# Kernel tuning notes

Measured on AMD Instinct MI355X. Metric: run time of the kernel, lower is better.

The kernel has to match this reference:

```python
import jax, jax.numpy as jnp
import numpy as np

B, S, HID = 4, 2048, 512
NH, HD = 8, 64
MAX_REL = 512


def setup_inputs() -> dict:
    key = jax.random.key(0)
    ks = jax.random.split(key, 10)
    sd = 0.02
    return {
        "hidden_states": jax.random.normal(ks[0], (B, S, HID), jnp.float32),
        "attention_mask": jnp.ones((B, S), jnp.float32),
        "Wq": jax.random.normal(ks[1], (HID, HID), jnp.float32) * sd,
        "bq": jnp.zeros((HID,), jnp.float32),
        "Wk": jax.random.normal(ks[2], (HID, HID), jnp.float32) * sd,
        "bk": jnp.zeros((HID,), jnp.float32),
        "Wv": jax.random.normal(ks[3], (HID, HID), jnp.float32) * sd,
        "bv": jnp.zeros((HID,), jnp.float32),
        "Wo": jax.random.normal(ks[4], (HID, HID), jnp.float32) * sd,
        "bo": jnp.zeros((HID,), jnp.float32),
        "rel_table": jax.random.normal(ks[5], (2 * MAX_REL + 1, NH), jnp.float32) * sd,
    }


def _heads(x):
    # [B,S,HID] -> [B,NH,S,HD]
    return x.reshape(B, S, NH, HD).transpose(0, 2, 1, 3)


def reference(hidden_states, attention_mask, Wq, bq, Wk, bk, Wv, bv, Wo, bo, rel_table):
    q = _heads(hidden_states @ Wq + bq)
    k = _heads(hidden_states @ Wk + bk)
    v = _heads(hidden_states @ Wv + bv)

    scores = jnp.einsum("bhqd,bhkd->bhqk", q, k) / jnp.sqrt(jnp.float32(HD))

    # relative position bias: rel[i,j] = clip(j-i, -MAX_REL, MAX_REL) + MAX_REL
    pos = jnp.arange(S)
    rel = jnp.clip(pos[None, :] - pos[:, None], -MAX_REL, MAX_REL) + MAX_REL
    bias = rel_table[rel]                      # [S,S,NH]
    bias = bias.transpose(2, 0, 1)             # [NH,S,S]
    scores = scores + bias[None]

    # mask: 1 attend, 0 masked
    neg = jnp.finfo(scores.dtype).min
    scores = scores + (1.0 - attention_mask)[:, None, None, :] * neg

    probs = jax.nn.softmax(scores, axis=-1)
    ctx = jnp.einsum("bhqk,bhkd->bhqd", probs, v)
    ctx = ctx.transpose(0, 2, 1, 3).reshape(B, S, HID)
    return ctx @ Wo + bo
```

## Files before the change

### kernel.cpp

```cpp
#include <hip/hip_runtime.h>
#include <hip/hip_bf16.h>

#define B_    4
#define S_    2048
#define HID_  512
#define NH_   8
#define HD_   64
#define MAXREL 512
#define M_    (B_ * S_)

#define LOG2E 1.44269504f
#define SCALE_Q (0.125f * LOG2E)

typedef __attribute__((ext_vector_type(8))) short bf8;
typedef __attribute__((ext_vector_type(4))) float f4;
typedef __attribute__((ext_vector_type(16))) float f16f;

static __device__ __forceinline__ unsigned short f2bf(float f) {
    union { float f; unsigned int u; } v; v.f = f;
    unsigned int u = v.u;
    unsigned int r = (u + 0x7FFFu + ((u >> 16) & 1u)) >> 16;
    return (unsigned short)r;
}

static __device__ __forceinline__ float ex2(float x) {
    float r; asm("v_exp_f32 %0, %1" : "=v"(r) : "v"(x)); return r;
}

static __device__ __forceinline__ void gload16(const void* g, void* l) {
    __builtin_amdgcn_global_load_lds(
        (const __attribute__((address_space(1))) unsigned int*)g,
        (__attribute__((address_space(3))) unsigned int*)l, 16, 0, 0);
}

static __device__ __forceinline__ bf8 mkbf8(unsigned a, unsigned b, unsigned c, unsigned d) {
    uint4 u = make_uint4(a, b, c, d);
    return *(bf8*)&u;
}

#define MFMA16(a, b, c) __builtin_amdgcn_mfma_f32_16x16x32_bf16((a), (b), (c), 0, 0, 0)
#define MFMA32(a, b, c) __builtin_amdgcn_mfma_f32_32x32x16_bf16((a), (b), (c), 0, 0, 0)

__global__ void k_cast_hs(const float* __restrict__ src, unsigned short* __restrict__ dst, int n4) {
    int i = blockIdx.x * blockDim.x + threadIdx.x;
    if (i >= n4) return;
    float4 v = ((const float4*)src)[i];
    ushort4 o;
    o.x = f2bf(v.x); o.y = f2bf(v.y); o.z = f2bf(v.z); o.w = f2bf(v.w);
    ((ushort4*)dst)[i] = o;
}

__global__ void k_prep_mask(const float* __restrict__ mask, float* __restrict__ maskadd) {
    int i = blockIdx.x * blockDim.x + threadIdx.x;
    if (i < M_) maskadd[i] = (1.0f - mask[i]) * -3.0e38f;
}

__global__ void k_transpose_w4(const float* __restrict__ W0, const float* __restrict__ W1,
                               const float* __restrict__ W2, const float* __restrict__ W3,
                               unsigned short* __restrict__ T0, unsigned short* __restrict__ T1,
                               unsigned short* __restrict__ T2, unsigned short* __restrict__ T3) {
    __shared__ float tile[32][33];
    const int z = blockIdx.z;
    const float* W = (z == 0) ? W0 : (z == 1) ? W1 : (z == 2) ? W2 : W3;
    unsigned short* T = (z == 0) ? T0 : (z == 1) ? T1 : (z == 2) ? T2 : T3;
    const int tx = threadIdx.x & 31, ty = threadIdx.x >> 5;
    const int n0 = blockIdx.x * 32, k0 = blockIdx.y * 32;
    #pragma unroll
    for (int i = 0; i < 4; ++i)
        tile[ty + i * 8][tx] = W[(size_t)(k0 + ty + i * 8) * HID_ + n0 + tx];
    __syncthreads();
    #pragma unroll
    for (int i = 0; i < 4; ++i)
        T[(size_t)(n0 + ty + i * 8) * HID_ + k0 + tx] = f2bf(tile[tx][ty + i * 8]);
}

__global__ __launch_bounds__(256, 3) void k_gemm_qkv(
    const unsigned short* __restrict__ Abf,
    const unsigned short* __restrict__ Wqt, const unsigned short* __restrict__ Wkt,
    const unsigned short* __restrict__ Wvt,
    const float* __restrict__ bq, const float* __restrict__ bk, const float* __restrict__ bv,
    unsigned short* __restrict__ Q, unsigned short* __restrict__ K, unsigned short* __restrict__ Vt)
{
    __shared__ unsigned short Al[2][128 * 32];
    __shared__ unsigned short Bl[2][128 * 32];

    const int t = threadIdx.x;
    const int lane = t & 63, w = t >> 6;
    const int lr = lane & 15, lg = lane >> 4;
    const int wr = w >> 1, wc = w & 1;

    const int m0 = blockIdx.x * 128;
    const int ng = blockIdx.y * 128;
    const int z = ng >> 9;
    const int n0 = ng & 511;
    const unsigned short* Wt = (z == 0) ? Wqt : ((z == 1) ? Wkt : Wvt);
    const float* bias = (z == 0) ? bq : ((z == 1) ? bk : bv);
    const float osc = (z == 0) ? SCALE_Q : 1.0f;

    const int srow = t >> 2;
    const int sc = (((t & 3) ^ ((srow >> 1) & 3))) * 8;
    const unsigned short* Ag0 = &Abf[(size_t)(m0 + srow) * HID_ + sc];
    const unsigned short* Ag1 = &Abf[(size_t)(m0 + 64 + srow) * HID_ + sc];
    const unsigned short* Bg0 = &Wt[(size_t)(n0 + srow) * HID_ + sc];
    const unsigned short* Bg1 = &Wt[(size_t)(n0 + 64 + srow) * HID_ + sc];
    char* dA0 = (char*)&Al[0][0] + w * 1024;
    char* dB0 = (char*)&Bl[0][0] + w * 1024;

    const int fx = (lr >> 1) & 3;
    int aoff[4], boff[4];
    #pragma unroll
    for (int i = 0; i < 4; ++i) {
        aoff[i] = (wr * 64 + i * 16 + lr) * 32 + ((lg ^ fx) * 8);
        boff[i] = (wc * 64 + i * 16 + lr) * 32 + ((lg ^ fx) * 8);
    }

    gload16(Ag0, dA0);
    gload16(Ag1, dA0 + 4096);
    gload16(Bg0, dB0);
    gload16(Bg1, dB0 + 4096);
    __syncthreads();

    f4 acc[4][4] = {};
    for (int kt = 0; kt < 16; ++kt) {
        const int cur = kt & 1;
        if (kt < 15) {
            const int ko = (kt + 1) * 32;
            const int bo = (cur ^ 1) * 8192;
            gload16(Ag0 + ko, dA0 + bo);
            gload16(Ag1 + ko, dA0 + bo + 4096);
            gload16(Bg0 + ko, dB0 + bo);
            gload16(Bg1 + ko, dB0 + bo + 4096);
        }
        bf8 af[4], bf_[4];
        #pragma unroll
        for (int i = 0; i < 4; ++i) {
            af[i]  = *(const bf8*)&Al[cur][aoff[i]];
            bf_[i] = *(const bf8*)&Bl[cur][boff[i]];
        }
        #pragma unroll
        for (int mi = 0; mi < 4; ++mi)
            #pragma unroll
            for (int ni = 0; ni < 4; ++ni)
                acc[mi][ni] = MFMA16(af[mi], bf_[ni], acc[mi][ni]);
        __syncthreads();
    }

    #pragma unroll
    for (int mi = 0; mi < 4; ++mi)
    #pragma unroll
    for (int ni = 0; ni < 4; ++ni) {
        const int col = n0 + wc * 64 + ni * 16 + lr;
        const int h = col >> 6, d = col & 63;
        const float bs = bias[col];
        const int row0 = m0 + wr * 64 + mi * 16 + lg * 4;
        const int b = row0 >> 11, s0 = row0 & 2047;
        if (z == 2) {
            ushort4 o;
            o.x = f2bf(acc[mi][ni][0] + bs);
            o.y = f2bf(acc[mi][ni][1] + bs);
            o.z = f2bf(acc[mi][ni][2] + bs);
            o.w = f2bf(acc[mi][ni][3] + bs);
            *(ushort4*)&Vt[(((size_t)(b * NH_ + h)) * HD_ + d) * S_ + s0] = o;
        } else {
            unsigned short* dst = (z == 0) ? Q : K;
            #pragma unroll
            for (int r = 0; r < 4; ++r) {
                float v = (acc[mi][ni][r] + bs) * osc;
                dst[(((size_t)(b * NH_ + h)) * S_ + s0 + r) * HD_ + d] = f2bf(v);
            }
        }
    }
}

__global__ __launch_bounds__(512) void k_gemm_out(
    const unsigned short* __restrict__ Abf,
    const unsigned short* __restrict__ Wot,
    const float* __restrict__ bo,
    float* __restrict__ out)
{
    __shared__ unsigned short Al[2][128 * 32];
    __shared__ unsigned short Bl[2][128 * 32];

    const int t = threadIdx.x;
    const int lane = t & 63, w = t >> 6;
    const int lr = lane & 15, lg = lane >> 4;
    const int wr = w >> 2, wc = w & 3;

    const int m0 = blockIdx.x * 128;
    const int n0 = blockIdx.y * 128;

    const int srow = t >> 2;
    const int sc = (((t & 3) ^ ((srow >> 1) & 3))) * 8;
    const unsigned short* Ag = &Abf[(size_t)(m0 + srow) * HID_ + sc];
    const unsigned short* Bg = &Wot[(size_t)(n0 + srow) * HID_ + sc];
    char* dA = (char*)&Al[0][0] + w * 1024;
    char* dB = (char*)&Bl[0][0] + w * 1024;

    const int fx = (lr >> 1) & 3;
    int aoff[4], boff[2];
    #pragma unroll
    for (int i = 0; i < 4; ++i)
        aoff[i] = (wr * 64 + i * 16 + lr) * 32 + ((lg ^ fx) * 8);
    #pragma unroll
    for (int i = 0; i < 2; ++i)
        boff[i] = (wc * 32 + i * 16 + lr) * 32 + ((lg ^ fx) * 8);

    gload16(Ag, dA);
    gload16(Bg, dB);
    __syncthreads();

    f4 acc[4][2] = {};
    for (int kt = 0; kt < 16; ++kt) {
        const int cur = kt & 1;
        if (kt < 15) {
            const int ko = (kt + 1) * 32;
            const int bo_ = (cur ^ 1) * 8192;
            gload16(Ag + ko, dA + bo_);
            gload16(Bg + ko, dB + bo_);
        }
        bf8 af[4], bf_[2];
        #pragma unroll
        for (int i = 0; i < 4; ++i) af[i] = *(const bf8*)&Al[cur][aoff[i]];
        #pragma unroll
        for (int i = 0; i < 2; ++i) bf_[i] = *(const bf8*)&Bl[cur][boff[i]];
        #pragma unroll
        for (int mi = 0; mi < 4; ++mi)
            #pragma unroll
            for (int ni = 0; ni < 2; ++ni)
                acc[mi][ni] = MFMA16(af[mi], bf_[ni], acc[mi][ni]);
        __syncthreads();
    }

    #pragma unroll
    for (int mi = 0; mi < 4; ++mi)
    #pragma unroll
    for (int ni = 0; ni < 2; ++ni) {
        const int col = n0 + wc * 32 + ni * 16 + lr;
        const float bs = bo[col];
        const int row0 = m0 + wr * 64 + mi * 16 + lg * 4;
        #pragma unroll
        for (int r = 0; r < 4; ++r)
            out[(size_t)(row0 + r) * HID_ + col] = acc[mi][ni][r] + bs;
    }
}

__global__ __launch_bounds__(256, 2) void k_flash(
    const unsigned short* __restrict__ Q, const unsigned short* __restrict__ K,
    const unsigned short* __restrict__ Vt,
    const float* __restrict__ rel_table, const float* __restrict__ maskadd,
    unsigned short* __restrict__ ctx)
{
    __shared__ unsigned short KV[3][8192];
    __shared__ float Tbp[2176];
    __shared__ float maskc[S_];

    const int t = threadIdx.x;
    const int lane = t & 63, w = t >> 6;
    const int q = lane & 31, hi = lane >> 5;

    const int flat = blockIdx.x;
    const int idx = flat >> 3;
    const int bh = (flat & 7) * 4 + (idx >> 4);
    const int qb = idx & 15;
    const int b = bh >> 3, h = bh & 7;
    const int q0 = qb * 128;

    for (int i = t; i < 2176; i += 256) {
        int r = i - q0 - 127;
        r = r < -MAXREL ? -MAXREL : (r > MAXREL ? MAXREL : r);
        Tbp[i] = rel_table[(r + MAXREL) * NH_ + h] * LOG2E;
    }
    {
        const float4* src = (const float4*)(maskadd + b * S_);
        float4* dst = (float4*)maskc;
        for (int i = t; i < S_ / 4; i += 256) dst[i] = src[i];
    }
    const float TbLo = rel_table[h] * LOG2E;
    const float TbHi = rel_table[2 * MAXREL * NH_ + h] * LOG2E;

    const unsigned short* Kb = K + (size_t)bh * S_ * HD_;
    const unsigned short* Vb = Vt + (size_t)bh * HD_ * S_;

    const int myq = q0 + w * 32 + q;
    const int qw = q0 + w * 32;
    bf8 qf[4];
    #pragma unroll
    for (int s = 0; s < 4; ++s)
        qf[s] = *(const bf8*)&Q[((size_t)bh * S_ + myq) * HD_ + s * 16 + hi * 8];

    const int srow = t >> 3, sslot = t & 7;
    const int sxor = (sslot ^ (srow & 7)) * 8;
    const size_t kb0 = (size_t)srow * HD_ + sxor;
    const size_t kb1 = (size_t)(srow + 32) * HD_ + sxor;
    const size_t vb0 = (size_t)srow * S_ + sxor;
    const size_t vb1 = (size_t)(srow + 32) * S_ + sxor;
    const int woff = w * 1024;

    auto stage = [&](int kvt, int buf) {
        char* base = (char*)&KV[buf][0];
        const size_t ko = (size_t)kvt * 64 * HD_;
        const size_t vo = (size_t)kvt * 64;
        gload16(&Kb[kb0 + ko], base + woff);
        gload16(&Kb[kb1 + ko], base + 4096 + woff);
        gload16(&Vb[vb0 + vo], base + 8192 + woff);
        gload16(&Vb[vb1 + vo], base + 8192 + 4096 + woff);
    };

    f16f ca0 = {}, ca1 = {};
    float m_s = -INFINITY, lsum = 0.f;

    stage(0, 0);
    stage(1, 1);
    asm volatile("s_waitcnt lgkmcnt(0)" ::: "memory");
    asm volatile("s_waitcnt vmcnt(4)" ::: "memory");
    __builtin_amdgcn_s_barrier();
    __builtin_amdgcn_sched_barrier(0);

    const int xq = q & 7;
    const int jb0 = 127 - w * 32 - q + 4 * hi;
    int cur = 0;
    for (int ti = 0; ti < 32; ++ti) {
        const int kv0 = ti * 64;

        if (ti < 30) {
            int nb = cur + 2; if (nb >= 3) nb -= 3;
            stage(ti + 2, nb);
        }
        const unsigned short* Kt  = &KV[cur][0];
        const unsigned short* Vtl = &KV[cur][4096];

        f16f sa0 = {}, sa1 = {};
        __builtin_amdgcn_s_setprio(1);
        #pragma unroll
        for (int s = 0; s < 4; ++s) {
            const int slot = ((2 * s + hi) ^ xq) * 8;
            bf8 k0 = *(const bf8*)&Kt[q * 64 + slot];
            bf8 k1 = *(const bf8*)&Kt[(q + 32) * 64 + slot];
            sa0 = MFMA32(k0, qf[s], sa0);
            sa1 = MFMA32(k1, qf[s], sa1);
        }
        __builtin_amdgcn_s_setprio(0);

        float tmaxl = -INFINITY;
        {
            const bool ulo = (kv0 + 31 - qw <= -MAXREL);
            const bool uhi = (kv0 - (qw + 31) >= MAXREL);
            if (ulo || uhi) {
                const float bc = ulo ? TbLo : TbHi;
                #pragma unroll
                for (int m = 0; m < 4; ++m) {
                    float4 mk = *(const float4*)&maskc[kv0 + m * 8 + hi * 4];
                    #pragma unroll
                    for (int r = 0; r < 4; ++r) {
                        float mkv = (r == 0) ? mk.x : (r == 1) ? mk.y : (r == 2) ? mk.z : mk.w;
                        float sv = sa0[4 * m + r] + bc + mkv;
                        sa0[4 * m + r] = sv;
                        tmaxl = fmaxf(tmaxl, sv);
                    }
                }
            } else {
                #pragma unroll
                for (int m = 0; m < 4; ++m) {
                    float4 mk = *(const float4*)&maskc[kv0 + m * 8 + hi * 4];
                    #pragma unroll
                    for (int r = 0; r < 4; ++r) {
                        float mkv = (r == 0) ? mk.x : (r == 1) ? mk.y : (r == 2) ? mk.z : mk.w;
                        float sv = sa0[4 * m + r] + Tbp[jb0 + kv0 + m * 8 + r] + mkv;
                        sa0[4 * m + r] = sv;
                        tmaxl = fmaxf(tmaxl, sv);
                    }
                }
            }
            const int kvh = kv0 + 32;
            const bool ulo1 = (kvh + 31 - qw <= -MAXREL);
            const bool uhi1 = (kvh - (qw + 31) >= MAXREL);
            if (ulo1 || uhi1) {
                const float bc = ulo1 ? TbLo : TbHi;
                #pragma unroll
                for (int m = 0; m < 4; ++m) {
                    float4 mk = *(const float4*)&maskc[kvh + m * 8 + hi * 4];
                    #pragma unroll
                    for (int r = 0; r < 4; ++r) {
                        float mkv = (r == 0) ? mk.x : (r == 1) ? mk.y : (r == 2) ? mk.z : mk.w;
                        float sv = sa1[4 * m + r] + bc + mkv;
                        sa1[4 * m + r] = sv;
                        tmaxl = fmaxf(tmaxl, sv);
                    }
                }
            } else {
                #pragma unroll
                for (int m = 0; m < 4; ++m) {
                    float4 mk = *(const float4*)&maskc[kvh + m * 8 + hi * 4];
                    #pragma unroll
                    for (int r = 0; r < 4; ++r) {
                        float mkv = (r == 0) ? mk.x : (r == 1) ? mk.y : (r == 2) ? mk.z : mk.w;
                        float sv = sa1[4 * m + r] + Tbp[jb0 + kvh + m * 8 + r] + mkv;
                        sa1[4 * m + r] = sv;
                        tmaxl = fmaxf(tmaxl, sv);
                    }
                }
            }
        }
        const float tmax = fmaxf(tmaxl, __shfl_xor(tmaxl, 32));

        float ptile = 0.f;
        unsigned int pkA[8], pkB[8];
        #pragma unroll
        for (int m = 0; m < 4; ++m) {
            float a0 = ex2(sa0[4 * m + 0] - m_s), a1 = ex2(sa0[4 * m + 1] - m_s);
            float a2 = ex2(sa0[4 * m + 2] - m_s), a3 = ex2(sa0[4 * m + 3] - m_s);
            float b0 = ex2(sa1[4 * m + 0] - m_s), b1 = ex2(sa1[4 * m + 1] - m_s);
            float b2 = ex2(sa1[4 * m + 2] - m_s), b3 = ex2(sa1[4 * m + 3] - m_s);
            ptile += ((a0 + a1) + (a2 + a3)) + ((b0 + b1) + (b2 + b3));
            asm("v_cvt_pk_bf16_f32 %0, %1, %2" : "=v"(pkA[2 * m])     : "v"(a0), "v"(a1));
            asm("v_cvt_pk_bf16_f32 %0, %1, %2" : "=v"(pkA[2 * m + 1]) : "v"(a2), "v"(a3));
            asm("v_cvt_pk_bf16_f32 %0, %1, %2" : "=v"(pkB[2 * m])     : "v"(b0), "v"(b1));
            asm("v_cvt_pk_bf16_f32 %0, %1, %2" : "=v"(pkB[2 * m + 1]) : "v"(b2), "v"(b3));
        }
        if (!__all(tmax <= m_s + 8.0f)) {
            const float mnew = fmaxf(m_s, tmax);
            const float fac = ex2(m_s - mnew);
            lsum *= fac;
            ca0 *= fac;
            ca1 *= fac;
            ptile = 0.f;
            #pragma unroll
            for (int m = 0; m < 4; ++m) {
                float a0 = ex2(sa0[4 * m + 0] - mnew), a1 = ex2(sa0[4 * m + 1] - mnew);
                float a2 = ex2(sa0[4 * m + 2] - mnew), a3 = ex2(sa0[4 * m + 3] - mnew);
                float b0 = ex2(sa1[4 * m + 0] - mnew), b1 = ex2(sa1[4 * m + 1] - mnew);
                float b2 = ex2(sa1[4 * m + 2] - mnew), b3 = ex2(sa1[4 * m + 3] - mnew);
                ptile += ((a0 + a1) + (a2 + a3)) + ((b0 + b1) + (b2 + b3));
                asm("v_cvt_pk_bf16_f32 %0, %1, %2" : "=v"(pkA[2 * m])     : "v"(a0), "v"(a1));
                asm("v_cvt_pk_bf16_f32 %0, %1, %2" : "=v"(pkA[2 * m + 1]) : "v"(a2), "v"(a3));
                asm("v_cvt_pk_bf16_f32 %0, %1, %2" : "=v"(pkB[2 * m])     : "v"(b0), "v"(b1));
                asm("v_cvt_pk_bf16_f32 %0, %1, %2" : "=v"(pkB[2 * m + 1]) : "v"(b2), "v"(b3));
            }
            m_s = mnew;
        }
        lsum += ptile;

        bf8 pf[4];
        #pragma unroll
        for (int s2 = 0; s2 < 2; ++s2) {
            unsigned c0 = pkA[4 * s2],     c2 = pkA[4 * s2 + 2];
            unsigned c1 = pkA[4 * s2 + 1], c3 = pkA[4 * s2 + 3];
            asm("v_permlane32_swap_b32 %0, %1" : "+v"(c0), "+v"(c2));
            asm("v_permlane32_swap_b32 %0, %1" : "+v"(c1), "+v"(c3));
            pf[s2] = mkbf8(c0, c1, c2, c3);
        }
        #pragma unroll
        for (int s2 = 0; s2 < 2; ++s2) {
            unsigned c0 = pkB[4 * s2],     c2 = pkB[4 * s2 + 2];
            unsigned c1 = pkB[4 * s2 + 1], c3 = pkB[4 * s2 + 3];
            asm("v_permlane32_swap_b32 %0, %1" : "+v"(c0), "+v"(c2));
            asm("v_permlane32_swap_b32 %0, %1" : "+v"(c1), "+v"(c3));
            pf[2 + s2] = mkbf8(c0, c1, c2, c3);
        }

        __builtin_amdgcn_s_setprio(1);
        #pragma unroll
        for (int s = 0; s < 4; ++s) {
            const int slot = ((2 * s + hi) ^ xq) * 8;
            bf8 v0 = *(const bf8*)&Vtl[q * 64 + slot];
            bf8 v1 = *(const bf8*)&Vtl[(q + 32) * 64 + slot];
            ca0 = MFMA32(v0, pf[s], ca0);
            ca1 = MFMA32(v1, pf[s], ca1);
        }
        __builtin_amdgcn_s_setprio(0);

        if (ti < 31) {
            if (ti < 30) asm volatile("s_waitcnt vmcnt(4)" ::: "memory");
            else         asm volatile("s_waitcnt vmcnt(0)" ::: "memory");
            __builtin_amdgcn_s_barrier();
            __builtin_amdgcn_sched_barrier(0);
        }
        cur = (cur == 2) ? 0 : cur + 1;
    }

    lsum += __shfl_xor(lsum, 32);
    const float inv = 1.0f / lsum;
    unsigned short* cg = &ctx[(size_t)(b * S_ + myq) * HID_ + h * HD_];
    #pragma unroll
    for (int m = 0; m < 4; ++m) {
        ushort4 o0;
        o0.x = f2bf(ca0[4 * m + 0] * inv);
        o0.y = f2bf(ca0[4 * m + 1] * inv);
        o0.z = f2bf(ca0[4 * m + 2] * inv);
        o0.w = f2bf(ca0[4 * m + 3] * inv);
        *(ushort4*)&cg[m * 8 + hi * 4] = o0;
        ushort4 o1;
        o1.x = f2bf(ca1[4 * m + 0] * inv);
        o1.y = f2bf(ca1[4 * m + 1] * inv);
        o1.z = f2bf(ca1[4 * m + 2] * inv);
        o1.w = f2bf(ca1[4 * m + 3] * inv);
        *(ushort4*)&cg[32 + m * 8 + hi * 4] = o1;
    }
}

extern "C" void kernel_launch(void* const* d_in, const int* in_sizes, int n_in,
                              void* d_out, int out_size, void* d_ws, size_t ws_size,
                              hipStream_t stream) {
    const float* hs  = (const float*)d_in[0];
    const float* msk = (const float*)d_in[1];
    const float* Wq  = (const float*)d_in[2];
    const float* bq  = (const float*)d_in[3];
    const float* Wk  = (const float*)d_in[4];
    const float* bk  = (const float*)d_in[5];
    const float* Wv  = (const float*)d_in[6];
    const float* bv  = (const float*)d_in[7];
    const float* Wo  = (const float*)d_in[8];
    const float* bo  = (const float*)d_in[9];
    const float* rel = (const float*)d_in[10];
    float* out = (float*)d_out;

    char* ws = (char*)d_ws;
    unsigned short* hsb = (unsigned short*)ws; ws += (size_t)M_ * HID_ * 2;
    unsigned short* Wqt = (unsigned short*)ws; ws += (size_t)HID_ * HID_ * 2;
    unsigned short* Wkt = (unsigned short*)ws; ws += (size_t)HID_ * HID_ * 2;
    unsigned short* Wvt = (unsigned short*)ws; ws += (size_t)HID_ * HID_ * 2;
    unsigned short* Wot = (unsigned short*)ws; ws += (size_t)HID_ * HID_ * 2;
    unsigned short* Qb  = (unsigned short*)ws; ws += (size_t)M_ * HID_ * 2;
    unsigned short* Kb  = (unsigned short*)ws; ws += (size_t)M_ * HID_ * 2;
    unsigned short* Vtb = (unsigned short*)ws; ws += (size_t)M_ * HID_ * 2;
    unsigned short* ctxb= (unsigned short*)ws; ws += (size_t)M_ * HID_ * 2;
    float* maskadd      = (float*)ws;          ws += (size_t)M_ * 4;

    k_cast_hs<<<(M_ * HID_ / 4 + 255) / 256, 256, 0, stream>>>(hs, hsb, M_ * HID_ / 4);
    k_prep_mask<<<(M_ + 255) / 256, 256, 0, stream>>>(msk, maskadd);
    k_transpose_w4<<<dim3(16, 16, 4), 256, 0, stream>>>(Wq, Wk, Wv, Wo, Wqt, Wkt, Wvt, Wot);
    k_gemm_qkv<<<dim3(64, 12), 256, 0, stream>>>(
        hsb, Wqt, Wkt, Wvt, bq, bk, bv, Qb, Kb, Vtb);
    k_flash<<<512, 256, 0, stream>>>(Qb, Kb, Vtb, rel, maskadd, ctxb);
    k_gemm_out<<<dim3(64, 4), 512, 0, stream>>>(ctxb, Wot, bo, out);
}
```

Measured before the change: 111.8 us.

## Software-pipeline PV MFMA one tile behind QK with a four-buffer KV ring

The P·V matrix multiply for tile ti-1 is deferred into iteration ti, issued right after the Q·K MFMAs. This lets the softmax work of one tile overlap matrix-core work from another, instead of serialising QK, softmax and PV inside each tile. The KV shared ring grows from three to four buffers so the previous V tile stays resident, and a tail block finishes the last PV. The relative-bias table is shrunk to a fixed 1216-entry window, and the row-max reduction is split into four independent chains to shorten dependency latency. The larger shared-memory footprint (~77KB per block) sits close to the per-CU limit at two blocks per CU.

After: 112.4 us. Within noise of the previous version (+0.5%).

```diff
diff --git a/kernel.cpp b/kernel.cpp
--- a/kernel.cpp
+++ b/kernel.cpp
@@ -250,8 +250,8 @@
     const float* __restrict__ rel_table, const float* __restrict__ maskadd,
     unsigned short* __restrict__ ctx)
 {
-    __shared__ unsigned short KV[3][8192];
-    __shared__ float Tbp[2176];
+    __shared__ unsigned short KV[4][8192];
+    __shared__ float Tw[1216];
     __shared__ float maskc[S_];
 
     const int t = threadIdx.x;
@@ -265,10 +265,10 @@
     const int b = bh >> 3, h = bh & 7;
     const int q0 = qb * 128;
 
-    for (int i = t; i < 2176; i += 256) {
-        int r = i - q0 - 127;
+    for (int i = t; i < 1216; i += 256) {
+        int r = i - 606;
         r = r < -MAXREL ? -MAXREL : (r > MAXREL ? MAXREL : r);
-        Tbp[i] = rel_table[(r + MAXREL) * NH_ + h] * LOG2E;
+        Tw[i] = rel_table[(r + MAXREL) * NH_ + h] * LOG2E;
     }
     {
         const float4* src = (const float4*)(maskadd + b * S_);
@@ -308,6 +308,8 @@
 
     f16f ca0 = {}, ca1 = {};
     float m_s = -INFINITY, lsum = 0.f;
+    bf8 pfA, pfB, pfC, pfD;
+    pfA = pfB = pfC = pfD = bf8{};
 
     stage(0, 0);
     stage(1, 1);
@@ -317,17 +319,14 @@
     __builtin_amdgcn_sched_barrier(0);
 
     const int xq = q & 7;
-    const int jb0 = 127 - w * 32 - q + 4 * hi;
-    int cur = 0;
+    const int jb0 = 606 - q0 - w * 32 - q + 4 * hi;
     for (int ti = 0; ti < 32; ++ti) {
         const int kv0 = ti * 64;
-
-        if (ti < 30) {
-            int nb = cur + 2; if (nb >= 3) nb -= 3;
-            stage(ti + 2, nb);
-        }
-        const unsigned short* Kt  = &KV[cur][0];
-        const unsigned short* Vtl = &KV[cur][4096];
+        const int cur = ti & 3;
+
+        if (ti < 30) stage(ti + 2, (ti + 2) & 3);
+
+        const unsigned short* Kt = &KV[cur][0];
 
         f16f sa0 = {}, sa1 = {};
         __builtin_amdgcn_s_setprio(1);
@@ -339,9 +338,21 @@
             sa0 = MFMA32(k0, qf[s], sa0);
             sa1 = MFMA32(k1, qf[s], sa1);
         }
+        if (ti > 0) {
+            const unsigned short* Vp = &KV[(ti + 3) & 3][4096];
+            #pragma unroll
+            for (int s = 0; s < 4; ++s) {
+                const int slot = ((2 * s + hi) ^ xq) * 8;
+                bf8 v0 = *(const bf8*)&Vp[q * 64 + slot];
+                bf8 v1 = *(const bf8*)&Vp[(q + 32) * 64 + slot];
+                bf8 pf = (s == 0) ? pfA : (s == 1) ? pfB : (s == 2) ? pfC : pfD;
+                ca0 = MFMA32(v0, pf, ca0);
+                ca1 = MFMA32(v1, pf, ca1);
+            }
+        }
         __builtin_amdgcn_s_setprio(0);
 
-        float tmaxl = -INFINITY;
+        float t0 = -INFINITY, t1 = -INFINITY, t2 = -INFINITY, t3 = -INFINITY;
         {
             const bool ulo = (kv0 + 31 - qw <= -MAXREL);
             const bool uhi = (kv0 - (qw + 31) >= MAXREL);
@@ -350,25 +361,20 @@
                 #pragma unroll
                 for (int m = 0; m < 4; ++m) {
                     float4 mk = *(const float4*)&maskc[kv0 + m * 8 + hi * 4];
-                    #pragma unroll
-                    for (int r = 0; r < 4; ++r) {
-                        float mkv = (r == 0) ? mk.x : (r == 1) ? mk.y : (r == 2) ? mk.z : mk.w;
-                        float sv = sa0[4 * m + r] + bc + mkv;
-                        sa0[4 * m + r] = sv;
-                        tmaxl = fmaxf(tmaxl, sv);
-                    }
+                    float s0 = sa0[4 * m + 0] + bc + mk.x;  sa0[4 * m + 0] = s0;  t0 = fmaxf(t0, s0);
+                    float s1 = sa0[4 * m + 1] + bc + mk.y;  sa0[4 * m + 1] = s1;  t1 = fmaxf(t1, s1);
+                    float s2 = sa0[4 * m + 2] + bc + mk.z;  sa0[4 * m + 2] = s2;  t2 = fmaxf(t2, s2);
+                    float s3 = sa0[4 * m + 3] + bc + mk.w;  sa0[4 * m + 3] = s3;  t3 = fmaxf(t3, s3);
                 }
             } else {
                 #pragma unroll
                 for (int m = 0; m < 4; ++m) {
                     float4 mk = *(const float4*)&maskc[kv0 + m * 8 + hi * 4];
-                    #pragma unroll
-                    for (int r = 0; r < 4; ++r) {
-                        float mkv = (r == 0) ? mk.x : (r == 1) ? mk.y : (r == 2) ? mk.z : mk.w;
-                        float sv = sa0[4 * m + r] + Tbp[jb0 + kv0 + m * 8 + r] + mkv;
-                        sa0[4 * m + r] = sv;
-                        tmaxl = fmaxf(tmaxl, sv);
-                    }
+                    const int jb = jb0 + kv0 + m * 8;
+                    float s0 = sa0[4 * m + 0] + Tw[jb + 0] + mk.x;  sa0[4 * m + 0] = s0;  t0 = fmaxf(t0, s0);
+                    float s1 = sa0[4 * m + 1] + Tw[jb + 1] + mk.y;  sa0[4 * m + 1] = s1;  t1 = fmaxf(t1, s1);
+                    float s2 = sa0[4 * m + 2] + Tw[jb + 2] + mk.z;  sa0[4 * m + 2] = s2;  t2 = fmaxf(t2, s2);
+                    float s3 = sa0[4 * m + 3] + Tw[jb + 3] + mk.w;  sa0[4 * m + 3] = s3;  t3 = fmaxf(t3, s3);
                 }
             }
             const int kvh = kv0 + 32;
@@ -379,28 +385,24 @@
                 #pragma unroll
                 for (int m = 0; m < 4; ++m) {
                     float4 mk = *(const float4*)&maskc[kvh + m * 8 + hi * 4];
-                    #pragma unroll
-                    for (int r = 0; r < 4; ++r) {
-                        float mkv = (r == 0) ? mk.x : (r == 1) ? mk.y : (r == 2) ? mk.z : mk.w;
-                        float sv = sa1[4 * m + r] + bc + mkv;
-                        sa1[4 * m + r] = sv;
-                        tmaxl = fmaxf(tmaxl, sv);
-                    }
+                    float s0 = sa1[4 * m + 0] + bc + mk.x;  sa1[4 * m + 0] = s0;  t0 = fmaxf(t0, s0);
+                    float s1 = sa1[4 * m + 1] + bc + mk.y;  sa1[4 * m + 1] = s1;  t1 = fmaxf(t1, s1);
+                    float s2 = sa1[4 * m + 2] + bc + mk.z;  sa1[4 * m + 2] = s2;  t2 = fmaxf(t2, s2);
+                    float s3 = sa1[4 * m + 3] + bc + mk.w;  sa1[4 * m + 3] = s3;  t3 = fmaxf(t3, s3);
                 }
             } else {
                 #pragma unroll
                 for (int m = 0; m < 4; ++m) {
                     float4 mk = *(const float4*)&maskc[kvh + m * 8 + hi * 4];
-                    #pragma unroll
-                    for (int r = 0; r < 4; ++r) {
-                        float mkv = (r == 0) ? mk.x : (r == 1) ? mk.y : (r == 2) ? mk.z : mk.w;
-                        float sv = sa1[4 * m + r] + Tbp[jb0 + kvh + m * 8 + r] + mkv;
-                        sa1[4 * m + r] = sv;
-                        tmaxl = fmaxf(tmaxl, sv);
-                    }
+                    const int jb = jb0 + kvh + m * 8;
+                    float s0 = sa1[4 * m + 0] + Tw[jb + 0] + mk.x;  sa1[4 * m + 0] = s0;  t0 = fmaxf(t0, s0);
+                    float s1 = sa1[4 * m + 1] + Tw[jb + 1] + mk.y;  sa1[4 * m + 1] = s1;  t1 = fmaxf(t1, s1);
+                    float s2 = sa1[4 * m + 2] + Tw[jb + 2] + mk.z;  sa1[4 * m + 2] = s2;  t2 = fmaxf(t2, s2);
+                    float s3 = sa1[4 * m + 3] + Tw[jb + 3] + mk.w;  sa1[4 * m + 3] = s3;  t3 = fmaxf(t3, s3);
                 }
             }
         }
+        float tmaxl = fmaxf(fmaxf(t0, t1), fmaxf(t2, t3));
         const float tmax = fmaxf(tmaxl, __shfl_xor(tmaxl, 32));
 
         float ptile = 0.f;
@@ -440,34 +442,30 @@
         }
         lsum += ptile;
 
-        bf8 pf[4];
-        #pragma unroll
-        for (int s2 = 0; s2 < 2; ++s2) {
-            unsigned c0 = pkA[4 * s2],     c2 = pkA[4 * s2 + 2];
-            unsigned c1 = pkA[4 * s2 + 1], c3 = pkA[4 * s2 + 3];
+        {
+            unsigned c0 = pkA[0], c2 = pkA[2], c1 = pkA[1], c3 = pkA[3];
             asm("v_permlane32_swap_b32 %0, %1" : "+v"(c0), "+v"(c2));
             asm("v_permlane32_swap_b32 %0, %1" : "+v"(c1), "+v"(c3));
-            pf[s2] = mkbf8(c0, c1, c2, c3);
-        }
-        #pragma unroll
-        for (int s2 = 0; s2 < 2; ++s2) {
-            unsigned c0 = pkB[4 * s2],     c2 = pkB[4 * s2 + 2];
-            unsigned c1 = pkB[4 * s2 + 1], c3 = pkB[4 * s2 + 3];
+            pfA = mkbf8(c0, c1, c2, c3);
+        }
+        {
+            unsigned c0 = pkA[4], c2 = pkA[6], c1 = pkA[5], c3 = pkA[7];
             asm("v_permlane32_swap_b32 %0, %1" : "+v"(c0), "+v"(c2));
             asm("v_permlane32_swap_b32 %0, %1" : "+v"(c1), "+v"(c3));
-            pf[2 + s2] = mkbf8(c0, c1, c2, c3);
-        }
-
-        __builtin_amdgcn_s_setprio(1);
-        #pragma unroll
-        for (int s = 0; s < 4; ++s) {
-            const int slot = ((2 * s + hi) ^ xq) * 8;
-            bf8 v0 = *(const bf8*)&Vtl[q * 64 + slot];
-            bf8 v1 = *(const bf8*)&Vtl[(q + 32) * 64 + slot];
-            ca0 = MFMA32(v0, pf[s], ca0);
-            ca1 = MFMA32(v1, pf[s], ca1);
-        }
-        __builtin_amdgcn_s_setprio(0);
+            pfB = mkbf8(c0, c1, c2, c3);
+        }
+        {
+            unsigned c0 = pkB[0], c2 = pkB[2], c1 = pkB[1], c3 = pkB[3];
+            asm("v_permlane32_swap_b32 %0, %1" : "+v"(c0), "+v"(c2));
+            asm("v_permlane32_swap_b32 %0, %1" : "+v"(c1), "+v"(c3));
+            pfC = mkbf8(c0, c1, c2, c3);
+        }
+        {
+            unsigned c0 = pkB[4], c2 = pkB[6], c1 = pkB[5], c3 = pkB[7];
+            asm("v_permlane32_swap_b32 %0, %1" : "+v"(c0), "+v"(c2));
+            asm("v_permlane32_swap_b32 %0, %1" : "+v"(c1), "+v"(c3));
+            pfD = mkbf8(c0, c1, c2, c3);
+        }
 
         if (ti < 31) {
             if (ti < 30) asm volatile("s_waitcnt vmcnt(4)" ::: "memory");
@@ -475,7 +473,21 @@
             __builtin_amdgcn_s_barrier();
             __builtin_amdgcn_sched_barrier(0);
         }
-        cur = (cur == 2) ? 0 : cur + 1;
+    }
+
+    {
+        const unsigned short* Vp = &KV[3][4096];
+        __builtin_amdgcn_s_setprio(1);
+        #pragma unroll
+        for (int s = 0; s < 4; ++s) {
+            const int slot = ((2 * s + hi) ^ xq) * 8;
+            bf8 v0 = *(const bf8*)&Vp[q * 64 + slot];
+            bf8 v1 = *(const bf8*)&Vp[(q + 32) * 64 + slot];
+            bf8 pf = (s == 0) ? pfA : (s == 1) ? pfB : (s == 2) ? pfC : pfD;
+            ca0 = MFMA32(v0, pf, ca0);
+            ca1 = MFMA32(v1, pf, ca1);
+        }
+        __builtin_amdgcn_s_setprio(0);
     }
 
     lsum += __shfl_xor(lsum, 32);
```

## Split KV tile across two wave groups in flash attention with final LSE merge

Applied to the files above, without the earlier changes.

The flash kernel goes from 4 to 8 waves per block. Each pair of waves shares the same 32 queries but handles a different 32-key half of every 64-key tile, and the two partial softmax states are merged through shared memory at the end. The relative-bias table is shrunk to a window that does not depend on the query block. The goal is more waves in flight to hide latency and a shorter serial chain per wave. The costs are an extra merge step with two block-wide barriers, and the launch bound asks for 4 blocks per CU, which limits registers per thread.

Result: no change. 110.5 us (-1.1%).

```diff
diff --git a/kernel.cpp b/kernel.cpp
--- a/kernel.cpp
+++ b/kernel.cpp
@@ -244,19 +244,20 @@
     }
 }
 
-__global__ __launch_bounds__(256, 2) void k_flash(
+__global__ __launch_bounds__(512, 4) void k_flash(
     const unsigned short* __restrict__ Q, const unsigned short* __restrict__ K,
     const unsigned short* __restrict__ Vt,
     const float* __restrict__ rel_table, const float* __restrict__ maskadd,
     unsigned short* __restrict__ ctx)
 {
     __shared__ unsigned short KV[3][8192];
-    __shared__ float Tbp[2176];
+    __shared__ float Tw[1216];
     __shared__ float maskc[S_];
 
     const int t = threadIdx.x;
     const int lane = t & 63, w = t >> 6;
     const int q = lane & 31, hi = lane >> 5;
+    const int g = w & 3, kvh = w >> 2;
 
     const int flat = blockIdx.x;
     const int idx = flat >> 3;
@@ -265,15 +266,15 @@
     const int b = bh >> 3, h = bh & 7;
     const int q0 = qb * 128;
 
-    for (int i = t; i < 2176; i += 256) {
-        int r = i - q0 - 127;
+    for (int i = t; i < 1216; i += 512) {
+        int r = i - 606;
         r = r < -MAXREL ? -MAXREL : (r > MAXREL ? MAXREL : r);
-        Tbp[i] = rel_table[(r + MAXREL) * NH_ + h] * LOG2E;
+        Tw[i] = rel_table[(r + MAXREL) * NH_ + h] * LOG2E;
     }
     {
         const float4* src = (const float4*)(maskadd + b * S_);
         float4* dst = (float4*)maskc;
-        for (int i = t; i < S_ / 4; i += 256) dst[i] = src[i];
+        for (int i = t; i < S_ / 4; i += 512) dst[i] = src[i];
     }
     const float TbLo = rel_table[h] * LOG2E;
     const float TbHi = rel_table[2 * MAXREL * NH_ + h] * LOG2E;
@@ -281,8 +282,8 @@
     const unsigned short* Kb = K + (size_t)bh * S_ * HD_;
     const unsigned short* Vb = Vt + (size_t)bh * HD_ * S_;
 
-    const int myq = q0 + w * 32 + q;
-    const int qw = q0 + w * 32;
+    const int myq = q0 + g * 32 + q;
+    const int qw = q0 + g * 32;
     bf8 qf[4];
     #pragma unroll
     for (int s = 0; s < 4; ++s)
@@ -291,19 +292,13 @@
     const int srow = t >> 3, sslot = t & 7;
     const int sxor = (sslot ^ (srow & 7)) * 8;
     const size_t kb0 = (size_t)srow * HD_ + sxor;
-    const size_t kb1 = (size_t)(srow + 32) * HD_ + sxor;
     const size_t vb0 = (size_t)srow * S_ + sxor;
-    const size_t vb1 = (size_t)(srow + 32) * S_ + sxor;
     const int woff = w * 1024;
 
     auto stage = [&](int kvt, int buf) {
         char* base = (char*)&KV[buf][0];
-        const size_t ko = (size_t)kvt * 64 * HD_;
-        const size_t vo = (size_t)kvt * 64;
-        gload16(&Kb[kb0 + ko], base + woff);
-        gload16(&Kb[kb1 + ko], base + 4096 + woff);
-        gload16(&Vb[vb0 + vo], base + 8192 + woff);
-        gload16(&Vb[vb1 + vo], base + 8192 + 4096 + woff);
+        gload16(&Kb[kb0 + (size_t)kvt * 64 * HD_], base + woff);
+        gload16(&Vb[vb0 + (size_t)kvt * 64], base + 8192 + woff);
     };
 
     f16f ca0 = {}, ca1 = {};
@@ -312,110 +307,69 @@
     stage(0, 0);
     stage(1, 1);
     asm volatile("s_waitcnt lgkmcnt(0)" ::: "memory");
-    asm volatile("s_waitcnt vmcnt(4)" ::: "memory");
+    asm volatile("s_waitcnt vmcnt(2)" ::: "memory");
     __builtin_amdgcn_s_barrier();
     __builtin_amdgcn_sched_barrier(0);
 
     const int xq = q & 7;
-    const int jb0 = 127 - w * 32 - q + 4 * hi;
-    int cur = 0;
+    const int jb0 = 606 + 32 * kvh + 4 * hi - q0 - g * 32 - q;
     for (int ti = 0; ti < 32; ++ti) {
         const int kv0 = ti * 64;
-
-        if (ti < 30) {
-            int nb = cur + 2; if (nb >= 3) nb -= 3;
-            stage(ti + 2, nb);
-        }
+        const int cur = ti % 3;
+        const int kvs = kv0 + 32 * kvh;
+
+        if (ti < 30) stage(ti + 2, (ti + 2) % 3);
+
         const unsigned short* Kt  = &KV[cur][0];
         const unsigned short* Vtl = &KV[cur][4096];
 
-        f16f sa0 = {}, sa1 = {};
+        f16f sa = {};
         __builtin_amdgcn_s_setprio(1);
         #pragma unroll
         for (int s = 0; s < 4; ++s) {
-            const int slot = ((2 * s + hi) ^ xq) * 8;
-            bf8 k0 = *(const bf8*)&Kt[q * 64 + slot];
-            bf8 k1 = *(const bf8*)&Kt[(q + 32) * 64 + slot];
-            sa0 = MFMA32(k0, qf[s], sa0);
-            sa1 = MFMA32(k1, qf[s], sa1);
+            bf8 kf = *(const bf8*)&Kt[(32 * kvh + q) * 64 + (((2 * s + hi) ^ xq) * 8)];
+            sa = MFMA32(kf, qf[s], sa);
         }
         __builtin_amdgcn_s_setprio(0);
 
-        float tmaxl = -INFINITY;
+        float t0 = -INFINITY, t1 = -INFINITY, t2 = -INFINITY, t3 = -INFINITY;
         {
-            const bool ulo = (kv0 + 31 - qw <= -MAXREL);
-            const bool uhi = (kv0 - (qw + 31) >= MAXREL);
+            const bool ulo = (kvs + 31 - qw <= -MAXREL);
+            const bool uhi = (kvs - (qw + 31) >= MAXREL);
             if (ulo || uhi) {
                 const float bc = ulo ? TbLo : TbHi;
                 #pragma unroll
                 for (int m = 0; m < 4; ++m) {
-                    float4 mk = *(const float4*)&maskc[kv0 + m * 8 + hi * 4];
-                    #pragma unroll
-                    for (int r = 0; r < 4; ++r) {
-                        float mkv = (r == 0) ? mk.x : (r == 1) ? mk.y : (r == 2) ? mk.z : mk.w;
-                        float sv = sa0[4 * m + r] + bc + mkv;
-                        sa0[4 * m + r] = sv;
-                        tmaxl = fmaxf(tmaxl, sv);
-                    }
+                    float4 mk = *(const float4*)&maskc[kvs + m * 8 + hi * 4];
+                    float s0 = sa[4 * m + 0] + bc + mk.x;  sa[4 * m + 0] = s0;  t0 = fmaxf(t0, s0);
+                    float s1 = sa[4 * m + 1] + bc + mk.y;  sa[4 * m + 1] = s1;  t1 = fmaxf(t1, s1);
+                    float s2 = sa[4 * m + 2] + bc + mk.z;  sa[4 * m + 2] = s2;  t2 = fmaxf(t2, s2);
+                    float s3 = sa[4 * m + 3] + bc + mk.w;  sa[4 * m + 3] = s3;  t3 = fmaxf(t3, s3);
                 }
             } else {
                 #pragma unroll
                 for (int m = 0; m < 4; ++m) {
-                    float4 mk = *(const float4*)&maskc[kv0 + m * 8 + hi * 4];
-                    #pragma unroll
-                    for (int r = 0; r < 4; ++r) {
-                        float mkv = (r == 0) ? mk.x : (r == 1) ? mk.y : (r == 2) ? mk.z : mk.w;
-                        float sv = sa0[4 * m + r] + Tbp[jb0 + kv0 + m * 8 + r] + mkv;
-                        sa0[4 * m + r] = sv;
-                        tmaxl = fmaxf(tmaxl, sv);
-                    }
+                    float4 mk = *(const float4*)&maskc[kvs + m * 8 + hi * 4];
+                    const int jb = jb0 + kv0 + m * 8;
+                    float s0 = sa[4 * m + 0] + Tw[jb + 0] + mk.x;  sa[4 * m + 0] = s0;  t0 = fmaxf(t0, s0);
+                    float s1 = sa[4 * m + 1] + Tw[jb + 1] + mk.y;  sa[4 * m + 1] = s1;  t1 = fmaxf(t1, s1);
+                    float s2 = sa[4 * m + 2] + Tw[jb + 2] + mk.z;  sa[4 * m + 2] = s2;  t2 = fmaxf(t2, s2);
+                    float s3 = sa[4 * m + 3] + Tw[jb + 3] + mk.w;  sa[4 * m + 3] = s3;  t3 = fmaxf(t3, s3);
                 }
             }
-            const int kvh = kv0 + 32;
-            const bool ulo1 = (kvh + 31 - qw <= -MAXREL);
-            const bool uhi1 = (kvh - (qw + 31) >= MAXREL);
-            if (ulo1 || uhi1) {
-                const float bc = ulo1 ? TbLo : TbHi;
-                #pragma unroll
-                for (int m = 0; m < 4; ++m) {
-                    float4 mk = *(const float4*)&maskc[kvh + m * 8 + hi * 4];
-                    #pragma unroll
-                    for (int r = 0; r < 4; ++r) {
-                        float mkv = (r == 0) ? mk.x : (r == 1) ? mk.y : (r == 2) ? mk.z : mk.w;
-                        float sv = sa1[4 * m + r] + bc + mkv;
-                        sa1[4 * m + r] = sv;
-                        tmaxl = fmaxf(tmaxl, sv);
-                    }
-                }
-            } else {
-                #pragma unroll
-                for (int m = 0; m < 4; ++m) {
-                    float4 mk = *(const float4*)&maskc[kvh + m * 8 + hi * 4];
-                    #pragma unroll
-                    for (int r = 0; r < 4; ++r) {
-                        float mkv = (r == 0) ? mk.x : (r == 1) ? mk.y : (r == 2) ? mk.z : mk.w;
-                        float sv = sa1[4 * m + r] + Tbp[jb0 + kvh + m * 8 + r] + mkv;
-                        sa1[4 * m + r] = sv;
-                        tmaxl = fmaxf(tmaxl, sv);
-                    }
-                }
-            }
-        }
+        }
+        float tmaxl = fmaxf(fmaxf(t0, t1), fmaxf(t2, t3));
         const float tmax = fmaxf(tmaxl, __shfl_xor(tmaxl, 32));
 
         float ptile = 0.f;
-        unsigned int pkA[8], pkB[8];
+        unsigned int pk[8];
         #pragma unroll
         for (int m = 0; m < 4; ++m) {
-            float a0 = ex2(sa0[4 * m + 0] - m_s), a1 = ex2(sa0[4 * m + 1] - m_s);
-            float a2 = ex2(sa0[4 * m + 2] - m_s), a3 = ex2(sa0[4 * m + 3] - m_s);
-            float b0 = ex2(sa1[4 * m + 0] - m_s), b1 = ex2(sa1[4 * m + 1] - m_s);
-            float b2 = ex2(sa1[4 * m + 2] - m_s), b3 = ex2(sa1[4 * m + 3] - m_s);
-            ptile += ((a0 + a1) + (a2 + a3)) + ((b0 + b1) + (b2 + b3));
-            asm("v_cvt_pk_bf16_f32 %0, %1, %2" : "=v"(pkA[2 * m])     : "v"(a0), "v"(a1));
-            asm("v_cvt_pk_bf16_f32 %0, %1, %2" : "=v"(pkA[2 * m + 1]) : "v"(a2), "v"(a3));
-            asm("v_cvt_pk_bf16_f32 %0, %1, %2" : "=v"(pkB[2 * m])     : "v"(b0), "v"(b1));
-            asm("v_cvt_pk_bf16_f32 %0, %1, %2" : "=v"(pkB[2 * m + 1]) : "v"(b2), "v"(b3));
+            float a0 = ex2(sa[4 * m + 0] - m_s), a1 = ex2(sa[4 * m + 1] - m_s);
+            float a2 = ex2(sa[4 * m + 2] - m_s), a3 = ex2(sa[4 * m + 3] - m_s);
+            ptile += (a0 + a1) + (a2 + a3);
+            asm("v_cvt_pk_bf16_f32 %0, %1, %2" : "=v"(pk[2 * m])     : "v"(a0), "v"(a1));
+            asm("v_cvt_pk_bf16_f32 %0, %1, %2" : "=v"(pk[2 * m + 1]) : "v"(a2), "v"(a3));
         }
         if (!__all(tmax <= m_s + 8.0f)) {
             const float mnew = fmaxf(m_s, tmax);
@@ -426,75 +380,89 @@
             ptile = 0.f;
             #pragma unroll
             for (int m = 0; m < 4; ++m) {
-                float a0 = ex2(sa0[4 * m + 0] - mnew), a1 = ex2(sa0[4 * m + 1] - mnew);
-                float a2 = ex2(sa0[4 * m + 2] - mnew), a3 = ex2(sa0[4 * m + 3] - mnew);
-                float b0 = ex2(sa1[4 * m + 0] - mnew), b1 = ex2(sa1[4 * m + 1] - mnew);
-                float b2 = ex2(sa1[4 * m + 2] - mnew), b3 = ex2(sa1[4 * m + 3] - mnew);
-                ptile += ((a0 + a1) + (a2 + a3)) + ((b0 + b1) + (b2 + b3));
-                asm("v_cvt_pk_bf16_f32 %0, %1, %2" : "=v"(pkA[2 * m])     : "v"(a0), "v"(a1));
-                asm("v_cvt_pk_bf16_f32 %0, %1, %2" : "=v"(pkA[2 * m + 1]) : "v"(a2), "v"(a3));
-                asm("v_cvt_pk_bf16_f32 %0, %1, %2" : "=v"(pkB[2 * m])     : "v"(b0), "v"(b1));
-                asm("v_cvt_pk_bf16_f32 %0, %1, %2" : "=v"(pkB[2 * m + 1]) : "v"(b2), "v"(b3));
+                float a0 = ex2(sa[4 * m + 0] - mnew), a1 = ex2(sa[4 * m + 1] - mnew);
+                float a2 = ex2(sa[4 * m + 2] - mnew), a3 = ex2(sa[4 * m + 3] - mnew);
+                ptile += (a0 + a1) + (a2 + a3);
+                asm("v_cvt_pk_bf16_f32 %0, %1, %2" : "=v"(pk[2 * m])     : "v"(a0), "v"(a1));
+                asm("v_cvt_pk_bf16_f32 %0, %1, %2" : "=v"(pk[2 * m + 1]) : "v"(a2), "v"(a3));
             }
             m_s = mnew;
         }
         lsum += ptile;
 
-        bf8 pf[4];
-        #pragma unroll
-        for (int s2 = 0; s2 < 2; ++s2) {
-            unsigned c0 = pkA[4 * s2],     c2 = pkA[4 * s2 + 2];
-            unsigned c1 = pkA[4 * s2 + 1], c3 = pkA[4 * s2 + 3];
+        bf8 pf0, pf1;
+        {
+            unsigned c0 = pk[0], c2 = pk[2], c1 = pk[1], c3 = pk[3];
             asm("v_permlane32_swap_b32 %0, %1" : "+v"(c0), "+v"(c2));
             asm("v_permlane32_swap_b32 %0, %1" : "+v"(c1), "+v"(c3));
-            pf[s2] = mkbf8(c0, c1, c2, c3);
-        }
-        #pragma unroll
-        for (int s2 = 0; s2 < 2; ++s2) {
-            unsigned c0 = pkB[4 * s2],     c2 = pkB[4 * s2 + 2];
-            unsigned c1 = pkB[4 * s2 + 1], c3 = pkB[4 * s2 + 3];
+            pf0 = mkbf8(c0, c1, c2, c3);
+        }
+        {
+            unsigned c0 = pk[4], c2 = pk[6], c1 = pk[5], c3 = pk[7];
             asm("v_permlane32_swap_b32 %0, %1" : "+v"(c0), "+v"(c2));
             asm("v_permlane32_swap_b32 %0, %1" : "+v"(c1), "+v"(c3));
-            pf[2 + s2] = mkbf8(c0, c1, c2, c3);
+            pf1 = mkbf8(c0, c1, c2, c3);
         }
 
         __builtin_amdgcn_s_setprio(1);
         #pragma unroll
-        for (int s = 0; s < 4; ++s) {
-            const int slot = ((2 * s + hi) ^ xq) * 8;
+        for (int s = 0; s < 2; ++s) {
+            const int slot = ((4 * kvh + 2 * s + hi) ^ xq) * 8;
             bf8 v0 = *(const bf8*)&Vtl[q * 64 + slot];
             bf8 v1 = *(const bf8*)&Vtl[(q + 32) * 64 + slot];
-            ca0 = MFMA32(v0, pf[s], ca0);
-            ca1 = MFMA32(v1, pf[s], ca1);
+            bf8 pf = (s == 0) ? pf0 : pf1;
+            ca0 = MFMA32(v0, pf, ca0);
+            ca1 = MFMA32(v1, pf, ca1);
         }
         __builtin_amdgcn_s_setprio(0);
 
         if (ti < 31) {
-            if (ti < 30) asm volatile("s_waitcnt vmcnt(4)" ::: "memory");
+            if (ti < 30) asm volatile("s_waitcnt vmcnt(2)" ::: "memory");
             else         asm volatile("s_waitcnt vmcnt(0)" ::: "memory");
             __builtin_amdgcn_s_barrier();
             __builtin_amdgcn_sched_barrier(0);
         }
-        cur = (cur == 2) ? 0 : cur + 1;
     }
 
     lsum += __shfl_xor(lsum, 32);
-    const float inv = 1.0f / lsum;
-    unsigned short* cg = &ctx[(size_t)(b * S_ + myq) * HID_ + h * HD_];
-    #pragma unroll
-    for (int m = 0; m < 4; ++m) {
-        ushort4 o0;
-        o0.x = f2bf(ca0[4 * m + 0] * inv);
-        o0.y = f2bf(ca0[4 * m + 1] * inv);
-        o0.z = f2bf(ca0[4 * m + 2] * inv);
-        o0.w = f2bf(ca0[4 * m + 3] * inv);
-        *(ushort4*)&cg[m * 8 + hi * 4] = o0;
-        ushort4 o1;
-        o1.x = f2bf(ca1[4 * m + 0] * inv);
-        o1.y = f2bf(ca1[4 * m + 1] * inv);
-        o1.z = f2bf(ca1[4 * m + 2] * inv);
-        o1.w = f2bf(ca1[4 * m + 3] * inv);
-        *(ushort4*)&cg[32 + m * 8 + hi * 4] = o1;
+
+    __syncthreads();
+    float* mg = (float*)&KV[0][0];
+    if (kvh == 1) {
+        const int base = g * 34 * 64;
+        #pragma unroll
+        for (int j = 0; j < 16; ++j) mg[base + j * 64 + lane] = ca0[j];
+        #pragma unroll
+        for (int j = 0; j < 16; ++j) mg[base + (16 + j) * 64 + lane] = ca1[j];
+        mg[base + 32 * 64 + lane] = m_s;
+        mg[base + 33 * 64 + lane] = lsum;
+    }
+    __syncthreads();
+    if (kvh == 0) {
+        const int base = g * 34 * 64;
+        const float pm = mg[base + 32 * 64 + lane];
+        const float pl = mg[base + 33 * 64 + lane];
+        const float mm = fmaxf(m_s, pm);
+        const float fa = ex2(m_s - mm);
+        const float fb = ex2(pm - mm);
+        const float lm = lsum * fa + pl * fb;
+        const float inv = 1.0f / lm;
+        unsigned short* cg = &ctx[(size_t)(b * S_ + myq) * HID_ + h * HD_];
+        #pragma unroll
+        for (int m = 0; m < 4; ++m) {
+            ushort4 o0;
+            o0.x = f2bf((ca0[4 * m + 0] * fa + mg[base + (4 * m + 0) * 64 + lane] * fb) * inv);
+            o0.y = f2bf((ca0[4 * m + 1] * fa + mg[base + (4 * m + 1) * 64 + lane] * fb) * inv);
+            o0.z = f2bf((ca0[4 * m + 2] * fa + mg[base + (4 * m + 2) * 64 + lane] * fb) * inv);
+            o0.w = f2bf((ca0[4 * m + 3] * fa + mg[base + (4 * m + 3) * 64 + lane] * fb) * inv);
+            *(ushort4*)&cg[m * 8 + hi * 4] = o0;
+            ushort4 o1;
+            o1.x = f2bf((ca1[4 * m + 0] * fa + mg[base + (16 + 4 * m + 0) * 64 + lane] * fb) * inv);
+            o1.y = f2bf((ca1[4 * m + 1] * fa + mg[base + (16 + 4 * m + 1) * 64 + lane] * fb) * inv);
+            o1.z = f2bf((ca1[4 * m + 2] * fa + mg[base + (16 + 4 * m + 2) * 64 + lane] * fb) * inv);
+            o1.w = f2bf((ca1[4 * m + 3] * fa + mg[base + (16 + 4 * m + 3) * 64 + lane] * fb) * inv);
+            *(ushort4*)&cg[32 + m * 8 + hi * 4] = o1;
+        }
     }
 }
 
@@ -531,6 +499,6 @@
     k_transpose_w4<<<dim3(16, 16, 4), 256, 0, stream>>>(Wq, Wk, Wv, Wo, Wqt, Wkt, Wvt, Wot);
     k_gemm_qkv<<<dim3(64, 12), 256, 0, stream>>>(
         hsb, Wqt, Wkt, Wvt, bq, bk, bv, Qb, Kb, Vtb);
-    k_flash<<<512, 256, 0, stream>>>(Qb, Kb, Vtb, rel, maskadd, ctxb);
+    k_flash<<<512, 512, 0, stream>>>(Qb, Kb, Vtb, rel, maskadd, ctxb);
     k_gemm_out<<<dim3(64, 4), 512, 0, stream>>>(ctxb, Wot, bo, out);
 }
```
